# Optimization experiments

Measured on AMD Instinct MI355X. Metric: run time of the kernel, lower is better.

Reference implementation:

```python
import jax, jax.numpy as jnp
import numpy as np

DIM = 512
HEADS = 8
DIM_HEAD = 64
INNER = HEADS * DIM_HEAD  # 512
EPS_LN = 1e-5
EPS_Q = 1e-6


def ternary_quant(w):
    # BitNet-style ternary quantization: scale by mean |w|, round to {-1,0,1}
    s = jnp.mean(jnp.abs(w))
    return jnp.round(jnp.clip(w / (s + EPS_Q), -1.0, 1.0)) * s


def layernorm(x, g, b):
    mu = jnp.mean(x, axis=-1, keepdims=True)
    var = jnp.mean(jnp.square(x - mu), axis=-1, keepdims=True)
    return (x - mu) * jax.lax.rsqrt(var + EPS_LN) * g + b


def setup_inputs() -> dict:
    key = jax.random.key(0)
    ks = jax.random.split(key, 6)
    x = jax.random.normal(ks[0], (8, 1024, DIM), dtype=jnp.float32)
    W_qkv = jax.random.normal(ks[1], (3 * INNER, DIM), dtype=jnp.float32) * (DIM ** -0.5)
    W_out = jax.random.normal(ks[2], (DIM, INNER), dtype=jnp.float32) * (INNER ** -0.5)
    b_out = jnp.zeros((DIM,), dtype=jnp.float32)
    g1 = jnp.ones((DIM,), dtype=jnp.float32)
    b1 = jnp.zeros((DIM,), dtype=jnp.float32)
    g2 = jnp.ones((INNER,), dtype=jnp.float32)
    b2 = jnp.zeros((INNER,), dtype=jnp.float32)
    return {"x": x, "g1": g1, "b1": b1, "W_qkv": W_qkv, "g2": g2, "b2": b2, "W_out": W_out, "b_out": b_out}


def reference(x, g1, b1, W_qkv, g2, b2, W_out, b_out):
    b, n, _ = x.shape
    scale = DIM_HEAD ** -0.5
    x = layernorm(x, g1, b1)
    qkv = x @ ternary_quant(W_qkv).T  # [b, n, 3*inner]
    q, k, v = jnp.split(qkv, 3, axis=-1)
    # b n (h d) -> b h n d
    def split_heads(t):
        return t.reshape(b, n, HEADS, DIM_HEAD).transpose(0, 2, 1, 3)
    q, k, v = split_heads(q), split_heads(k), split_heads(v)
    attn_map = jnp.einsum('bhnd,bhmd->bhnm', q, k) * scale  # [b,h,n,n]
    attn = jax.nn.softmax(attn_map, axis=-1)
    out = jnp.einsum('bhnm,bhmd->bhnd', attn, v)
    out = out.transpose(0, 2, 1, 3).reshape(b, n, INNER)  # b n (h d)
    out = layernorm(out, g2, b2)
    out = out @ ternary_quant(W_out).T + b_out
    return out
```

## Files before the change

kernel.cpp:

```cpp
#include <hip/hip_runtime.h>
#include <hip/hip_bf16.h>

typedef __bf16 bf16x8 __attribute__((ext_vector_type(8)));
typedef float  f32x4  __attribute__((ext_vector_type(4)));

#define SEQ   1024
#define BATCH 8
#define DIMM  512
#define HEADS 8
#define DHEAD 64
#define TRIPLE 1536
#define MROWS (BATCH*SEQ)

#define GLOAD_LDS16(g, l) __builtin_amdgcn_global_load_lds( \
    (const __attribute__((address_space(1))) void*)(const void*)(g), \
    (__attribute__((address_space(3))) void*)(void*)(l), 16, 0, 0)

__global__ __launch_bounds__(256) void absum_all(const float* __restrict__ w1,
                                                 const float* __restrict__ w2,
                                                 float* __restrict__ part) {
    const int bid = blockIdx.x, tid = threadIdx.x;
    float s = 0.f;
    if (bid < 256) {
        const float4* p = (const float4*)w1;
        for (int i = bid * 256 + tid; i < 196608; i += 65536) {
            float4 v = p[i];
            s += fabsf(v.x) + fabsf(v.y) + fabsf(v.z) + fabsf(v.w);
        }
    } else {
        const float4* p = (const float4*)w2;
        for (int i = (bid - 256) * 256 + tid; i < 65536; i += 16384) {
            float4 v = p[i];
            s += fabsf(v.x) + fabsf(v.y) + fabsf(v.z) + fabsf(v.w);
        }
    }
    for (int o = 32; o; o >>= 1) s += __shfl_down(s, o);
    __shared__ float red[4];
    if (!(tid & 63)) red[tid >> 6] = s;
    __syncthreads();
    if (tid == 0) part[bid] = red[0] + red[1] + red[2] + red[3];
}

__global__ void finalize_scales(const float* __restrict__ part, float* __restrict__ scales) {
    int t = threadIdx.x;
    float v1 = part[t];
    float v2 = (t < 64) ? part[256 + t] : 0.f;
    for (int o = 32; o; o >>= 1) { v1 += __shfl_down(v1, o); v2 += __shfl_down(v2, o); }
    __shared__ float r1[4], r2[4];
    int lane = t & 63, wv = t >> 6;
    if (!lane) { r1[wv] = v1; r2[wv] = v2; }
    __syncthreads();
    if (t == 0) {
        scales[0] = (r1[0] + r1[1] + r1[2] + r1[3]) / 786432.0f;
        scales[1] = (r2[0] + r2[1] + r2[2] + r2[3]) / 262144.0f;
    }
}

__global__ __launch_bounds__(256) void quant_all(const float* __restrict__ w1,
                                                 const float* __restrict__ w2,
                                                 const float* __restrict__ scp,
                                                 __bf16* __restrict__ o1,
                                                 __bf16* __restrict__ o2) {
    const int bid = blockIdx.x;
    const float* w; __bf16* o; float s; int idx;
    if (bid < 768) { w = w1; o = o1; s = scp[0]; idx = (bid * 256 + threadIdx.x) * 4; }
    else           { w = w2; o = o2; s = scp[1]; idx = ((bid - 768) * 256 + threadIdx.x) * 4; }
    const float inv = 1.f / (s + 1e-6f);
    float4 v = *reinterpret_cast<const float4*>(w + idx);
    o[idx + 0] = (__bf16)(rintf(fminf(1.f, fmaxf(-1.f, v.x * inv))) * s);
    o[idx + 1] = (__bf16)(rintf(fminf(1.f, fmaxf(-1.f, v.y * inv))) * s);
    o[idx + 2] = (__bf16)(rintf(fminf(1.f, fmaxf(-1.f, v.z * inv))) * s);
    o[idx + 3] = (__bf16)(rintf(fminf(1.f, fmaxf(-1.f, v.w * inv))) * s);
}

template<typename TIN>
__global__ __launch_bounds__(256) void ln_fast(const TIN* __restrict__ x,
                                               const float* __restrict__ g,
                                               const float* __restrict__ bta,
                                               __bf16* __restrict__ y) {
    const int row = blockIdx.x * 4 + (threadIdx.x >> 6);
    const int lane = threadIdx.x & 63;
    float v[8];
    if constexpr (sizeof(TIN) == 4) {
        const float4* xr = (const float4*)((const float*)x + (size_t)row * DIMM + lane * 8);
        float4 a = xr[0], bq = xr[1];
        v[0] = a.x; v[1] = a.y; v[2] = a.z; v[3] = a.w;
        v[4] = bq.x; v[5] = bq.y; v[6] = bq.z; v[7] = bq.w;
    } else {
        bf16x8 a = *reinterpret_cast<const bf16x8*>((const __bf16*)x + (size_t)row * DIMM + lane * 8);
#pragma unroll
        for (int e = 0; e < 8; ++e) v[e] = (float)a[e];
    }
    float s = 0.f, sq = 0.f;
#pragma unroll
    for (int e = 0; e < 8; ++e) { s += v[e]; sq += v[e] * v[e]; }
    for (int o = 32; o; o >>= 1) { s += __shfl_xor(s, o); sq += __shfl_xor(sq, o); }
    const float mu = s * (1.f / DIMM);
    const float invs = rsqrtf(sq * (1.f / DIMM) - mu * mu + 1e-5f);
    const float4* gp = (const float4*)(g + lane * 8);
    const float4* bp = (const float4*)(bta + lane * 8);
    float4 g0 = gp[0], g1 = gp[1], b0 = bp[0], b1 = bp[1];
    float o_[8] = {
        (v[0] - mu) * invs * g0.x + b0.x, (v[1] - mu) * invs * g0.y + b0.y,
        (v[2] - mu) * invs * g0.z + b0.z, (v[3] - mu) * invs * g0.w + b0.w,
        (v[4] - mu) * invs * g1.x + b1.x, (v[5] - mu) * invs * g1.y + b1.y,
        (v[6] - mu) * invs * g1.z + b1.z, (v[7] - mu) * invs * g1.w + b1.w };
    uint4 st;
    asm("v_cvt_pk_bf16_f32 %0, %1, %2" : "=v"(st.x) : "v"(o_[0]), "v"(o_[1]));
    asm("v_cvt_pk_bf16_f32 %0, %1, %2" : "=v"(st.y) : "v"(o_[2]), "v"(o_[3]));
    asm("v_cvt_pk_bf16_f32 %0, %1, %2" : "=v"(st.z) : "v"(o_[4]), "v"(o_[5]));
    asm("v_cvt_pk_bf16_f32 %0, %1, %2" : "=v"(st.w) : "v"(o_[6]), "v"(o_[7]));
    *reinterpret_cast<uint4*>(y + (size_t)row * DIMM + lane * 8) = st;
}

template<int NCOLS, bool BIAS, bool OUT_F32>
__global__ __launch_bounds__(256) void gemm_lds(const __bf16* __restrict__ A,
                                                const __bf16* __restrict__ Wt,
                                                const float* __restrict__ bias,
                                                __bf16* __restrict__ outb,
                                                float* __restrict__ outf) {
    const int K = DIMM;
    __shared__ __align__(16) __bf16 As[2][4096];
    __shared__ __align__(16) __bf16 Bs[2][4096];

    const int tid = threadIdx.x;
    const int w = tid >> 6, lane = tid & 63;
    const int m = lane & 15, g = lane >> 4;
    const int mi = w >> 1, ni = w & 1;

    const int trow = tid >> 2;
    const int tc = tid & 3;
    const int sc = (tc ^ ((trow >> 1) & 3)) * 8;
    const __bf16* a0 = A  + (size_t)(blockIdx.x * 128 + trow) * K + sc;
    const __bf16* a1 = a0 + (size_t)64 * K;
    const __bf16* b0 = Wt + (size_t)(blockIdx.y * 128 + trow) * K + sc;
    const __bf16* b1 = b0 + (size_t)64 * K;

    f32x4 acc[4][4] = {};

    GLOAD_LDS16(a0, (char*)As[0] + tid * 16);
    GLOAD_LDS16(a1, (char*)As[0] + 4096 + tid * 16);
    GLOAD_LDS16(b0, (char*)Bs[0] + tid * 16);
    GLOAD_LDS16(b1, (char*)Bs[0] + 4096 + tid * 16);

    int cur = 0;
    for (int k0 = 0; k0 < K; k0 += 32) {
        __syncthreads();
        if (k0 + 32 < K) {
            GLOAD_LDS16(a0 + k0 + 32, (char*)As[cur ^ 1] + tid * 16);
            GLOAD_LDS16(a1 + k0 + 32, (char*)As[cur ^ 1] + 4096 + tid * 16);
            GLOAD_LDS16(b0 + k0 + 32, (char*)Bs[cur ^ 1] + tid * 16);
            GLOAD_LDS16(b1 + k0 + 32, (char*)Bs[cur ^ 1] + 4096 + tid * 16);
        }

        const char* Ab = (const char*)As[cur];
        const char* Bb = (const char*)Bs[cur];
        bf16x8 af[4], bfr[4];
#pragma unroll
        for (int i = 0; i < 4; ++i) {
            const int ra = mi * 64 + i * 16 + m;
            af[i] = *reinterpret_cast<const bf16x8*>(Ab + ra * 64 + ((g ^ ((ra >> 1) & 3)) << 4));
        }
#pragma unroll
        for (int j = 0; j < 4; ++j) {
            const int rb = ni * 64 + j * 16 + m;
            bfr[j] = *reinterpret_cast<const bf16x8*>(Bb + rb * 64 + ((g ^ ((rb >> 1) & 3)) << 4));
        }
#pragma unroll
        for (int i = 0; i < 4; ++i)
#pragma unroll
            for (int j = 0; j < 4; ++j)
                acc[i][j] = __builtin_amdgcn_mfma_f32_16x16x32_bf16(af[i], bfr[j], acc[i][j], 0, 0, 0);
        cur ^= 1;
    }

    const int orow0 = blockIdx.x * 128 + mi * 64 + g * 4;
    const int ocol0 = blockIdx.y * 128 + ni * 64;
#pragma unroll
    for (int i = 0; i < 4; ++i)
#pragma unroll
        for (int j = 0; j < 4; ++j)
#pragma unroll
            for (int r = 0; r < 4; ++r) {
                int row = orow0 + i * 16 + r;
                int col = ocol0 + j * 16 + m;
                float v = acc[i][j][r];
                if (BIAS) v += bias[col];
                if (OUT_F32) outf[(size_t)row * NCOLS + col] = v;
                else         outb[(size_t)row * NCOLS + col] = (__bf16)v;
            }
}

__global__ __launch_bounds__(256, 2) void attn_mfma(const __bf16* __restrict__ qkv,
                                                    __bf16* __restrict__ out) {
    const int qt = blockIdx.y, bh = blockIdx.x;
    const int b = bh >> 3, h = bh & 7;
    const int tid = threadIdx.x;
    const int w = tid >> 6, lane = tid & 63;
    const int g = lane >> 4, m = lane & 15;

    __shared__ __align__(16) __bf16 Kb[4096];
    __shared__ __align__(16) __bf16 Vt[4096];
    __shared__ __align__(16) __bf16 Pl[4][2048];

    bf16x8 qf[2][2];
    {
        const __bf16* qp = qkv + (size_t)(b * SEQ + qt * 128 + w * 32 + m) * TRIPLE + h * 64 + g * 8;
#pragma unroll
        for (int hf = 0; hf < 2; ++hf) {
            qf[hf][0] = *reinterpret_cast<const bf16x8*>(qp + (size_t)hf * 16 * TRIPLE);
            qf[hf][1] = *reinterpret_cast<const bf16x8*>(qp + (size_t)hf * 16 * TRIPLE + 32);
#pragma unroll
            for (int e = 0; e < 8; ++e) {
                qf[hf][0][e] = (__bf16)((float)qf[hf][0][e] * 0.125f);
                qf[hf][1][e] = (__bf16)((float)qf[hf][1][e] * 0.125f);
            }
        }
    }

    const int srow = tid >> 3;
    const int sc   = tid & 7;
    const size_t rbase = (size_t)(b * SEQ + srow) * TRIPLE + h * 64 + sc * 8;
    const __bf16* k0s = qkv + rbase + DIMM;
    const __bf16* v0s = qkv + rbase + 2 * DIMM;
    const __bf16* k1s = k0s + (size_t)32 * TRIPLE;
    const __bf16* v1s = v0s + (size_t)32 * TRIPLE;
    const int kstep = 64 * TRIPLE;

    char* kw0 = (char*)Kb + srow * 128 + ((sc ^ (srow & 7)) << 4);
    char* kw1 = kw0 + 32 * 128;
    char* vbp = (char*)Vt;

    f32x4 oa[2][4] = {};
    float mrun[2] = {-1e30f, -1e30f}, lrun[2] = {0.f, 0.f};

    uint4 k0c = *reinterpret_cast<const uint4*>(k0s);
    uint4 k1c = *reinterpret_cast<const uint4*>(k1s);
    uint4 v0c = *reinterpret_cast<const uint4*>(v0s);
    uint4 v1c = *reinterpret_cast<const uint4*>(v1s);
    uint4 k0n = {}, k1n = {}, v0n = {}, v1n = {};

    for (int t = 0; t < 16; ++t) {
        __syncthreads();

        *reinterpret_cast<bf16x8*>(kw0) = *reinterpret_cast<bf16x8*>(&k0c);
        *reinterpret_cast<bf16x8*>(kw1) = *reinterpret_cast<bf16x8*>(&k1c);
        {
            bf16x8 va = *reinterpret_cast<bf16x8*>(&v0c);
            bf16x8 vb = *reinterpret_cast<bf16x8*>(&v1c);
#pragma unroll
            for (int e = 0; e < 8; ++e) {
                const int dro = (sc * 8 + e) * 128;
                const int sw = ((sc ^ e) & 7) << 4;
                *(__bf16*)(vbp + dro + ((srow * 2) ^ sw))        = va[e];
                *(__bf16*)(vbp + dro + (((srow + 32) * 2) ^ sw)) = vb[e];
            }
        }
        __syncthreads();

        if (t < 15) {
            k0n = *reinterpret_cast<const uint4*>(k0s + (size_t)(t + 1) * kstep);
            k1n = *reinterpret_cast<const uint4*>(k1s + (size_t)(t + 1) * kstep);
            v0n = *reinterpret_cast<const uint4*>(v0s + (size_t)(t + 1) * kstep);
            v1n = *reinterpret_cast<const uint4*>(v1s + (size_t)(t + 1) * kstep);
        }

        const char* kb = (const char*)Kb;
        f32x4 sa[2][4];
#pragma unroll
        for (int hf = 0; hf < 2; ++hf)
#pragma unroll
            for (int i = 0; i < 4; ++i) sa[hf][i] = (f32x4){0.f, 0.f, 0.f, 0.f};
#pragma unroll
        for (int kc = 0; kc < 2; ++kc) {
            const int cp = ((kc * 4 + g) ^ (m & 7)) << 4;
#pragma unroll
            for (int i = 0; i < 4; ++i) {
                bf16x8 kf = *reinterpret_cast<const bf16x8*>(kb + (i * 16 + m) * 128 + cp);
                sa[0][i] = __builtin_amdgcn_mfma_f32_16x16x32_bf16(kf, qf[0][kc], sa[0][i], 0, 0, 0);
                sa[1][i] = __builtin_amdgcn_mfma_f32_16x16x32_bf16(kf, qf[1][kc], sa[1][i], 0, 0, 0);
            }
        }

        char* pw = (char*)Pl[w] + m * 128;
        const int psw = (m & 7) << 4;
#pragma unroll
        for (int hf = 0; hf < 2; ++hf) {
            float mx = -1e30f;
#pragma unroll
            for (int i = 0; i < 4; ++i)
#pragma unroll
                for (int r = 0; r < 4; ++r) mx = fmaxf(mx, sa[hf][i][r]);
            mx = fmaxf(mx, __shfl_xor(mx, 16));
            mx = fmaxf(mx, __shfl_xor(mx, 32));
            const float mnew = fmaxf(mrun[hf], mx);
            float p[4][4];
            float ps = 0.f;
#pragma unroll
            for (int i = 0; i < 4; ++i)
#pragma unroll
                for (int r = 0; r < 4; ++r) { p[i][r] = __expf(sa[hf][i][r] - mnew); ps += p[i][r]; }
            ps += __shfl_xor(ps, 16);
            ps += __shfl_xor(ps, 32);
            const float al = __expf(mrun[hf] - mnew);
            mrun[hf] = mnew;
            lrun[hf] = lrun[hf] * al + ps;
#pragma unroll
            for (int i = 0; i < 4; ++i)
#pragma unroll
                for (int r = 0; r < 4; ++r) oa[hf][i][r] *= al;
#pragma unroll
            for (int i = 0; i < 4; ++i) {
                uint2 pk;
                asm("v_cvt_pk_bf16_f32 %0, %1, %2" : "=v"(pk.x) : "v"(p[i][0]), "v"(p[i][1]));
                asm("v_cvt_pk_bf16_f32 %0, %1, %2" : "=v"(pk.y) : "v"(p[i][2]), "v"(p[i][3]));
                *reinterpret_cast<uint2*>(pw + hf * 16 * 128 + ((i * 32 + g * 8) ^ psw)) = pk;
            }
        }

        bf16x8 pf[2][2];
#pragma unroll
        for (int hf = 0; hf < 2; ++hf)
#pragma unroll
            for (int kc = 0; kc < 2; ++kc)
                pf[hf][kc] = *reinterpret_cast<const bf16x8*>(
                    pw + hf * 16 * 128 + ((kc * 64 + g * 16) ^ psw));

#pragma unroll
        for (int kc = 0; kc < 2; ++kc)
#pragma unroll
            for (int i = 0; i < 4; ++i) {
                const int sv = ((i * 2 + (m >> 3)) ^ (m & 7)) & 7;
                bf16x8 vf = *reinterpret_cast<const bf16x8*>(
                    vbp + (i * 16 + m) * 128 + (((kc * 4 + g) ^ sv) << 4));
                oa[0][i] = __builtin_amdgcn_mfma_f32_16x16x32_bf16(vf, pf[0][kc], oa[0][i], 0, 0, 0);
                oa[1][i] = __builtin_amdgcn_mfma_f32_16x16x32_bf16(vf, pf[1][kc], oa[1][i], 0, 0, 0);
            }

        k0c = k0n; k1c = k1n; v0c = v0n; v1c = v1n;
    }

#pragma unroll
    for (int hf = 0; hf < 2; ++hf) {
        const float inv = 1.0f / lrun[hf];
        unsigned int* orow = (unsigned int*)(out +
            (size_t)(b * SEQ + qt * 128 + w * 32 + hf * 16 + m) * DIMM + h * 64);
#pragma unroll
        for (int i = 0; i < 4; ++i)
#pragma unroll
            for (int rp = 0; rp < 2; ++rp) {
                float o0 = oa[hf][i][2 * rp] * inv, o1 = oa[hf][i][2 * rp + 1] * inv;
                unsigned int pk;
                asm("v_cvt_pk_bf16_f32 %0, %1, %2" : "=v"(pk) : "v"(o0), "v"(o1));
                orow[i * 8 + g * 2 + rp] = pk;
            }
    }
}

extern "C" void kernel_launch(void* const* d_in, const int* in_sizes, int n_in,
                              void* d_out, int out_size, void* d_ws, size_t ws_size,
                              hipStream_t stream) {
    const float* x     = (const float*)d_in[0];
    const float* g1    = (const float*)d_in[1];
    const float* b1    = (const float*)d_in[2];
    const float* W_qkv = (const float*)d_in[3];
    const float* g2    = (const float*)d_in[4];
    const float* b2    = (const float*)d_in[5];
    const float* W_out = (const float*)d_in[6];
    const float* b_out = (const float*)d_in[7];
    float* out = (float*)d_out;

    char* ws = (char*)d_ws;
    float* part   = (float*)(ws);
    float* scales = (float*)(ws + 2048);
    __bf16* Wq1 = (__bf16*)(ws + 4096);
    __bf16* Wq2 = (__bf16*)(ws + 4096 + 1572864);
    __bf16* Xln = (__bf16*)(ws + 4096 + 1572864 + 524288);
    __bf16* QKV = (__bf16*)(ws + 4096 + 1572864 + 524288 + 8388608);
    __bf16* AO  = (__bf16*)(ws + 4096 + 1572864 + 524288 + 8388608 + 25165824);

    absum_all<<<320, 256, 0, stream>>>(W_qkv, W_out, part);
    finalize_scales<<<1, 256, 0, stream>>>(part, scales);
    quant_all<<<1024, 256, 0, stream>>>(W_qkv, W_out, scales, Wq1, Wq2);
    ln_fast<float><<<MROWS / 4, 256, 0, stream>>>(x, g1, b1, Xln);
    gemm_lds<TRIPLE, false, false><<<dim3(64, 12), 256, 0, stream>>>(Xln, Wq1, nullptr, QKV, nullptr);
    attn_mfma<<<dim3(64, 8), 256, 0, stream>>>(QKV, AO);
    ln_fast<__bf16><<<MROWS / 4, 256, 0, stream>>>(AO, g2, b2, Xln);
    gemm_lds<DIMM, true, true><<<dim3(64, 4), 256, 0, stream>>>(Xln, Wq2, b_out, nullptr, out);
}
```

Before: 89.86 us.

## Halve attention query tile to 64 rows and fold scale finalize into quant

The attention kernel now gives each block 64 query rows instead of 128, with one 16-row slice per wave. That doubles the grid to 1024 blocks and raises the occupancy hint to 4 blocks per CU. Separately, the single-block finalize_scales kernel is removed: every quant_all block re-reduces the partial sums itself, which saves one launch and a serial dependency. In exchange, K/V tiles are loaded from global memory and staged through LDS twice as often per query, and each wave does less MFMA work per LDS load.

```diff
diff --git a/kernel.cpp b/kernel.cpp
--- a/kernel.cpp
+++ b/kernel.cpp
@@ -41,31 +41,26 @@
     if (tid == 0) part[bid] = red[0] + red[1] + red[2] + red[3];
 }
 
-__global__ void finalize_scales(const float* __restrict__ part, float* __restrict__ scales) {
-    int t = threadIdx.x;
-    float v1 = part[t];
-    float v2 = (t < 64) ? part[256 + t] : 0.f;
-    for (int o = 32; o; o >>= 1) { v1 += __shfl_down(v1, o); v2 += __shfl_down(v2, o); }
-    __shared__ float r1[4], r2[4];
-    int lane = t & 63, wv = t >> 6;
-    if (!lane) { r1[wv] = v1; r2[wv] = v2; }
-    __syncthreads();
-    if (t == 0) {
-        scales[0] = (r1[0] + r1[1] + r1[2] + r1[3]) / 786432.0f;
-        scales[1] = (r2[0] + r2[1] + r2[2] + r2[3]) / 262144.0f;
-    }
-}
-
 __global__ __launch_bounds__(256) void quant_all(const float* __restrict__ w1,
                                                  const float* __restrict__ w2,
-                                                 const float* __restrict__ scp,
+                                                 const float* __restrict__ part,
                                                  __bf16* __restrict__ o1,
                                                  __bf16* __restrict__ o2) {
-    const int bid = blockIdx.x;
-    const float* w; __bf16* o; float s; int idx;
-    if (bid < 768) { w = w1; o = o1; s = scp[0]; idx = (bid * 256 + threadIdx.x) * 4; }
-    else           { w = w2; o = o2; s = scp[1]; idx = ((bid - 768) * 256 + threadIdx.x) * 4; }
+    const int bid = blockIdx.x, tid = threadIdx.x;
+    float acc = 0.f;
+    if (bid < 768) acc = part[tid];
+    else if (tid < 64) acc = part[256 + tid];
+    for (int o = 32; o; o >>= 1) acc += __shfl_down(acc, o);
+    __shared__ float red[4];
+    if (!(tid & 63)) red[tid >> 6] = acc;
+    __syncthreads();
+    const float tot = red[0] + red[1] + red[2] + red[3];
+    const float s = (bid < 768) ? tot / 786432.0f : tot / 262144.0f;
     const float inv = 1.f / (s + 1e-6f);
+
+    const float* w; __bf16* o; int idx;
+    if (bid < 768) { w = w1; o = o1; idx = (bid * 256 + tid) * 4; }
+    else           { w = w2; o = o2; idx = ((bid - 768) * 256 + tid) * 4; }
     float4 v = *reinterpret_cast<const float4*>(w + idx);
     o[idx + 0] = (__bf16)(rintf(fminf(1.f, fmaxf(-1.f, v.x * inv))) * s);
     o[idx + 1] = (__bf16)(rintf(fminf(1.f, fmaxf(-1.f, v.y * inv))) * s);
@@ -191,7 +186,7 @@
             }
 }
 
-__global__ __launch_bounds__(256, 2) void attn_mfma(const __bf16* __restrict__ qkv,
+__global__ __launch_bounds__(256, 4) void attn_mfma(const __bf16* __restrict__ qkv,
                                                     __bf16* __restrict__ out) {
     const int qt = blockIdx.y, bh = blockIdx.x;
     const int b = bh >> 3, h = bh & 7;
@@ -201,20 +196,17 @@
 
     __shared__ __align__(16) __bf16 Kb[4096];
     __shared__ __align__(16) __bf16 Vt[4096];
-    __shared__ __align__(16) __bf16 Pl[4][2048];
-
-    bf16x8 qf[2][2];
+    __shared__ __align__(16) __bf16 Pl[4][1024];
+
+    bf16x8 qf[2];
     {
-        const __bf16* qp = qkv + (size_t)(b * SEQ + qt * 128 + w * 32 + m) * TRIPLE + h * 64 + g * 8;
-#pragma unroll
-        for (int hf = 0; hf < 2; ++hf) {
-            qf[hf][0] = *reinterpret_cast<const bf16x8*>(qp + (size_t)hf * 16 * TRIPLE);
-            qf[hf][1] = *reinterpret_cast<const bf16x8*>(qp + (size_t)hf * 16 * TRIPLE + 32);
-#pragma unroll
-            for (int e = 0; e < 8; ++e) {
-                qf[hf][0][e] = (__bf16)((float)qf[hf][0][e] * 0.125f);
-                qf[hf][1][e] = (__bf16)((float)qf[hf][1][e] * 0.125f);
-            }
+        const __bf16* qp = qkv + (size_t)(b * SEQ + qt * 64 + w * 16 + m) * TRIPLE + h * 64 + g * 8;
+        qf[0] = *reinterpret_cast<const bf16x8*>(qp);
+        qf[1] = *reinterpret_cast<const bf16x8*>(qp + 32);
+#pragma unroll
+        for (int e = 0; e < 8; ++e) {
+            qf[0][e] = (__bf16)((float)qf[0][e] * 0.125f);
+            qf[1][e] = (__bf16)((float)qf[1][e] * 0.125f);
         }
     }
 
@@ -231,8 +223,8 @@
     char* kw1 = kw0 + 32 * 128;
     char* vbp = (char*)Vt;
 
-    f32x4 oa[2][4] = {};
-    float mrun[2] = {-1e30f, -1e30f}, lrun[2] = {0.f, 0.f};
+    f32x4 oa[4] = {};
+    float mrun = -1e30f, lrun = 0.f;
 
     uint4 k0c = *reinterpret_cast<const uint4*>(k0s);
     uint4 k1c = *reinterpret_cast<const uint4*>(k1s);
@@ -266,65 +258,58 @@
         }
 
         const char* kb = (const char*)Kb;
-        f32x4 sa[2][4];
-#pragma unroll
-        for (int hf = 0; hf < 2; ++hf)
-#pragma unroll
-            for (int i = 0; i < 4; ++i) sa[hf][i] = (f32x4){0.f, 0.f, 0.f, 0.f};
+        f32x4 sa[4];
+#pragma unroll
+        for (int i = 0; i < 4; ++i) sa[i] = (f32x4){0.f, 0.f, 0.f, 0.f};
 #pragma unroll
         for (int kc = 0; kc < 2; ++kc) {
             const int cp = ((kc * 4 + g) ^ (m & 7)) << 4;
 #pragma unroll
             for (int i = 0; i < 4; ++i) {
                 bf16x8 kf = *reinterpret_cast<const bf16x8*>(kb + (i * 16 + m) * 128 + cp);
-                sa[0][i] = __builtin_amdgcn_mfma_f32_16x16x32_bf16(kf, qf[0][kc], sa[0][i], 0, 0, 0);
-                sa[1][i] = __builtin_amdgcn_mfma_f32_16x16x32_bf16(kf, qf[1][kc], sa[1][i], 0, 0, 0);
+                sa[i] = __builtin_amdgcn_mfma_f32_16x16x32_bf16(kf, qf[kc], sa[i], 0, 0, 0);
             }
         }
 
         char* pw = (char*)Pl[w] + m * 128;
         const int psw = (m & 7) << 4;
-#pragma unroll
-        for (int hf = 0; hf < 2; ++hf) {
+        {
             float mx = -1e30f;
 #pragma unroll
             for (int i = 0; i < 4; ++i)
 #pragma unroll
-                for (int r = 0; r < 4; ++r) mx = fmaxf(mx, sa[hf][i][r]);
+                for (int r = 0; r < 4; ++r) mx = fmaxf(mx, sa[i][r]);
             mx = fmaxf(mx, __shfl_xor(mx, 16));
             mx = fmaxf(mx, __shfl_xor(mx, 32));
-            const float mnew = fmaxf(mrun[hf], mx);
+            const float mnew = fmaxf(mrun, mx);
             float p[4][4];
             float ps = 0.f;
 #pragma unroll
             for (int i = 0; i < 4; ++i)
 #pragma unroll
-                for (int r = 0; r < 4; ++r) { p[i][r] = __expf(sa[hf][i][r] - mnew); ps += p[i][r]; }
+                for (int r = 0; r < 4; ++r) { p[i][r] = __expf(sa[i][r] - mnew); ps += p[i][r]; }
             ps += __shfl_xor(ps, 16);
             ps += __shfl_xor(ps, 32);
-            const float al = __expf(mrun[hf] - mnew);
-            mrun[hf] = mnew;
-            lrun[hf] = lrun[hf] * al + ps;
+            const float al = __expf(mrun - mnew);
+            mrun = mnew;
+            lrun = lrun * al + ps;
 #pragma unroll
             for (int i = 0; i < 4; ++i)
 #pragma unroll
-                for (int r = 0; r < 4; ++r) oa[hf][i][r] *= al;
+                for (int r = 0; r < 4; ++r) oa[i][r] *= al;
 #pragma unroll
             for (int i = 0; i < 4; ++i) {
                 uint2 pk;
                 asm("v_cvt_pk_bf16_f32 %0, %1, %2" : "=v"(pk.x) : "v"(p[i][0]), "v"(p[i][1]));
                 asm("v_cvt_pk_bf16_f32 %0, %1, %2" : "=v"(pk.y) : "v"(p[i][2]), "v"(p[i][3]));
-                *reinterpret_cast<uint2*>(pw + hf * 16 * 128 + ((i * 32 + g * 8) ^ psw)) = pk;
-            }
-        }
-
-        bf16x8 pf[2][2];
-#pragma unroll
-        for (int hf = 0; hf < 2; ++hf)
-#pragma unroll
-            for (int kc = 0; kc < 2; ++kc)
-                pf[hf][kc] = *reinterpret_cast<const bf16x8*>(
-                    pw + hf * 16 * 128 + ((kc * 64 + g * 16) ^ psw));
+                *reinterpret_cast<uint2*>(pw + ((i * 32 + g * 8) ^ psw)) = pk;
+            }
+        }
+
+        bf16x8 pf[2];
+#pragma unroll
+        for (int kc = 0; kc < 2; ++kc)
+            pf[kc] = *reinterpret_cast<const bf16x8*>(pw + ((kc * 64 + g * 16) ^ psw));
 
 #pragma unroll
         for (int kc = 0; kc < 2; ++kc)
@@ -333,28 +318,24 @@
                 const int sv = ((i * 2 + (m >> 3)) ^ (m & 7)) & 7;
                 bf16x8 vf = *reinterpret_cast<const bf16x8*>(
                     vbp + (i * 16 + m) * 128 + (((kc * 4 + g) ^ sv) << 4));
-                oa[0][i] = __builtin_amdgcn_mfma_f32_16x16x32_bf16(vf, pf[0][kc], oa[0][i], 0, 0, 0);
-                oa[1][i] = __builtin_amdgcn_mfma_f32_16x16x32_bf16(vf, pf[1][kc], oa[1][i], 0, 0, 0);
+                oa[i] = __builtin_amdgcn_mfma_f32_16x16x32_bf16(vf, pf[kc], oa[i], 0, 0, 0);
             }
 
         k0c = k0n; k1c = k1n; v0c = v0n; v1c = v1n;
     }
 
-#pragma unroll
-    for (int hf = 0; hf < 2; ++hf) {
-        const float inv = 1.0f / lrun[hf];
-        unsigned int* orow = (unsigned int*)(out +
-            (size_t)(b * SEQ + qt * 128 + w * 32 + hf * 16 + m) * DIMM + h * 64);
-#pragma unroll
-        for (int i = 0; i < 4; ++i)
-#pragma unroll
-            for (int rp = 0; rp < 2; ++rp) {
-                float o0 = oa[hf][i][2 * rp] * inv, o1 = oa[hf][i][2 * rp + 1] * inv;
-                unsigned int pk;
-                asm("v_cvt_pk_bf16_f32 %0, %1, %2" : "=v"(pk) : "v"(o0), "v"(o1));
-                orow[i * 8 + g * 2 + rp] = pk;
-            }
-    }
+    const float inv = 1.0f / lrun;
+    unsigned int* orow = (unsigned int*)(out +
+        (size_t)(b * SEQ + qt * 64 + w * 16 + m) * DIMM + h * 64);
+#pragma unroll
+    for (int i = 0; i < 4; ++i)
+#pragma unroll
+        for (int rp = 0; rp < 2; ++rp) {
+            float o0 = oa[i][2 * rp] * inv, o1 = oa[i][2 * rp + 1] * inv;
+            unsigned int pk;
+            asm("v_cvt_pk_bf16_f32 %0, %1, %2" : "=v"(pk) : "v"(o0), "v"(o1));
+            orow[i * 8 + g * 2 + rp] = pk;
+        }
 }
 
 extern "C" void kernel_launch(void* const* d_in, const int* in_sizes, int n_in,
@@ -372,7 +353,6 @@
 
     char* ws = (char*)d_ws;
     float* part   = (float*)(ws);
-    float* scales = (float*)(ws + 2048);
     __bf16* Wq1 = (__bf16*)(ws + 4096);
     __bf16* Wq2 = (__bf16*)(ws + 4096 + 1572864);
     __bf16* Xln = (__bf16*)(ws + 4096 + 1572864 + 524288);
@@ -380,11 +360,10 @@
     __bf16* AO  = (__bf16*)(ws + 4096 + 1572864 + 524288 + 8388608 + 25165824);
 
     absum_all<<<320, 256, 0, stream>>>(W_qkv, W_out, part);
-    finalize_scales<<<1, 256, 0, stream>>>(part, scales);
-    quant_all<<<1024, 256, 0, stream>>>(W_qkv, W_out, scales, Wq1, Wq2);
+    quant_all<<<1024, 256, 0, stream>>>(W_qkv, W_out, part, Wq1, Wq2);
     ln_fast<float><<<MROWS / 4, 256, 0, stream>>>(x, g1, b1, Xln);
     gemm_lds<TRIPLE, false, false><<<dim3(64, 12), 256, 0, stream>>>(Xln, Wq1, nullptr, QKV, nullptr);
-    attn_mfma<<<dim3(64, 8), 256, 0, stream>>>(QKV, AO);
+    attn_mfma<<<dim3(64, 16), 256, 0, stream>>>(QKV, AO);
     ln_fast<__bf16><<<MROWS / 4, 256, 0, stream>>>(AO, g2, b2, Xln);
     gemm_lds<DIMM, true, true><<<dim3(64, 4), 256, 0, stream>>>(Xln, Wq2, b_out, nullptr, out);
 }
```

Result: no change. 89.82 us (-0.0%).
